# Optimization experiments

Hardware: AMD Instinct MI355X
Metric: run time of the kernel (lower is better)

Reference implementation:

```python
import jax, jax.numpy as jnp
import numpy as np

NTYPES = 4
RCUT = 6.0
MIXED_TYPES = False
BOX = 40.0  # Angstrom, sets realistic atomic density


def setup_inputs() -> dict:
    key = jax.random.key(0)
    k1, k2 = jax.random.split(key)
    nframes, nloc = 2, 4096
    coord = jax.random.uniform(k1, (nframes, nloc * 3), dtype=jnp.float32) * BOX
    atype = jax.random.randint(k2, (nframes, nloc), 0, NTYPES, dtype=jnp.int32)
    return {"coord": coord, "atype": atype}


def reference(coord, atype):
    # cell=None branch: extended coords == local coords, nall == nloc
    nframes = coord.shape[0]
    c = coord.reshape(nframes, -1, 3)              # (f, nloc, 3)
    nloc = c.shape[1]
    # diff[f, i, j] = coord[j] - coord[i], shape (f, nloc, nall, 3)
    diff = c[:, None, :, :] - c[:, :, None, :]
    rr2 = jnp.sum(diff * diff, axis=-1)            # (f, nloc, nall)
    # mask self-pairs with inf (torch sets diff rows to inf before squaring)
    eye = jnp.eye(nloc, dtype=bool)
    rr2 = jnp.where(eye[None, :, :], jnp.inf, rr2)
    min_rr2 = jnp.min(rr2, axis=-1)                # (f, nloc)
    mask = rr2 < RCUT ** 2                         # (f, nloc, nall)
    if not MIXED_TYPES:
        # per-type neighbor counts via one-hot contraction (replaces the
        # Python loop over ntypes in the torch code; same math)
        onehot = jax.nn.one_hot(atype, NTYPES, dtype=jnp.int32)  # (f, nall, t)
        nnei = jnp.einsum('fij,fjt->fit', mask.astype(jnp.int32), onehot)
    else:
        valid = (atype >= 0)[:, None, :]
        nnei = jnp.sum(mask & valid, axis=-1).astype(jnp.int32)[..., None]
    max_nnei = jnp.max(nnei, axis=1)               # (f, ntypes) or (f, 1)
    return min_rr2, max_nnei
```

## Files before the change

kernel.cpp:

```cpp
#include <hip/hip_runtime.h>
#include <stdint.h>

#define NFRAMES 2
#define NT 4
#define BLK 256
#define NJ 64

__global__ __launch_bounds__(BLK) void ns_init_kernel(unsigned* __restrict__ out_bits,
                                                      unsigned* __restrict__ ws, int n) {
    int idx = blockIdx.x * BLK + threadIdx.x;
    if (idx < n) {
        out_bits[idx] = 0x7F800000u;
        ws[idx] = 0u;
    }
}

template <bool SELFCHK>
__device__ __forceinline__ void do_pair(const float* __restrict__ cf,
                                        const int* __restrict__ tf,
                                        int j, int i,
                                        float xi, float yi, float zi,
                                        float& mm, unsigned& cc) {
#pragma clang fp contract(off)
    float dx = cf[3 * j]     - xi;
    float dy = cf[3 * j + 1] - yi;
    float dz = cf[3 * j + 2] - zi;
    unsigned sval = 1u << (tf[j] * 8);
    float xx = dx * dx;
    float yy = dy * dy;
    float zz = dz * dz;
    float r2 = (xx + yy) + zz;
    bool self = SELFCHK && (j == i);
    float rm = self ? __builtin_inff() : r2;
    mm = fminf(mm, rm);
    bool near = (r2 < 36.0f) && !self;
    cc += near ? sval : 0u;
}

__global__ __launch_bounds__(BLK) void ns_pair_kernel(const float* __restrict__ coord,
                                                      const int* __restrict__ atype,
                                                      unsigned* __restrict__ out_min_bits,
                                                      unsigned* __restrict__ ws_cnt,
                                                      int nloc) {
    const int f = blockIdx.z;
    const int ibase = blockIdx.y * BLK;
    const int i = ibase + threadIdx.x;
    const int jslice = nloc / NJ;
    const int jbase = blockIdx.x * jslice;

    const float* cf = coord + (size_t)f * nloc * 3;
    const int*   tf = atype + (size_t)f * nloc;

    const float xi = cf[3 * i];
    const float yi = cf[3 * i + 1];
    const float zi = cf[3 * i + 2];

    float m0 = __builtin_inff(), m1 = __builtin_inff();
    unsigned c0 = 0u, c1 = 0u;

    const bool overlap = (jbase >= ibase) && (jbase < ibase + BLK);

    if (overlap) {
#pragma unroll 8
        for (int j = jbase; j < jbase + jslice; j += 2) {
            do_pair<true>(cf, tf, j,     i, xi, yi, zi, m0, c0);
            do_pair<true>(cf, tf, j + 1, i, xi, yi, zi, m1, c1);
        }
    } else {
#pragma unroll 8
        for (int j = jbase; j < jbase + jslice; j += 2) {
            do_pair<false>(cf, tf, j,     i, xi, yi, zi, m0, c0);
            do_pair<false>(cf, tf, j + 1, i, xi, yi, zi, m1, c1);
        }
    }

    float minr2 = fminf(m0, m1);
    unsigned c = c0 + c1;

    atomicMin(&out_min_bits[(size_t)f * nloc + i], __float_as_uint(minr2));
    atomicAdd(&ws_cnt[(size_t)f * nloc + i], c);
}

__global__ __launch_bounds__(BLK) void ns_max_kernel(const unsigned* __restrict__ ws_cnt,
                                                     float* __restrict__ out,
                                                     int nloc) {
    const int f = blockIdx.x;
    int m0 = 0, m1 = 0, m2 = 0, m3 = 0;
    for (int i = threadIdx.x; i < nloc; i += BLK) {
        unsigned c = ws_cnt[(size_t)f * nloc + i];
        m0 = max(m0, (int)(c & 255u));
        m1 = max(m1, (int)((c >> 8) & 255u));
        m2 = max(m2, (int)((c >> 16) & 255u));
        m3 = max(m3, (int)(c >> 24));
    }
    for (int off = 32; off > 0; off >>= 1) {
        m0 = max(m0, __shfl_xor(m0, off, 64));
        m1 = max(m1, __shfl_xor(m1, off, 64));
        m2 = max(m2, __shfl_xor(m2, off, 64));
        m3 = max(m3, __shfl_xor(m3, off, 64));
    }
    __shared__ int red[BLK / 64][NT];
    int wid = threadIdx.x >> 6;
    if ((threadIdx.x & 63) == 0) {
        red[wid][0] = m0; red[wid][1] = m1; red[wid][2] = m2; red[wid][3] = m3;
    }
    __syncthreads();
    if (threadIdx.x < NT) {
        int t = threadIdx.x;
        int m = max(max(red[0][t], red[1][t]), max(red[2][t], red[3][t]));
        out[(size_t)NFRAMES * nloc + f * NT + t] = (float)m;
    }
}

extern "C" void kernel_launch(void* const* d_in, const int* in_sizes, int n_in,
                              void* d_out, int out_size, void* d_ws, size_t ws_size,
                              hipStream_t stream) {
    const float* coord = (const float*)d_in[0];
    const int*   atype = (const int*)d_in[1];
    const int nloc = in_sizes[1] / NFRAMES;

    float*    out = (float*)d_out;
    unsigned* ws  = (unsigned*)d_ws;

    const int n = NFRAMES * nloc;

    ns_init_kernel<<<(n + BLK - 1) / BLK, BLK, 0, stream>>>((unsigned*)out, ws, n);

    dim3 grid(NJ, nloc / BLK, NFRAMES);
    ns_pair_kernel<<<grid, dim3(BLK), 0, stream>>>(coord, atype, (unsigned*)out, ws, nloc);

    ns_max_kernel<<<NFRAMES, BLK, 0, stream>>>(ws, out, nloc);
}
```

Measured before the change: 27.56 us.

## Replace atomic accumulation with per-slice partial buffers and a parallel finalize

The pair kernel now writes each j-slice's partial min and packed per-type count to a workspace array instead of doing atomicMin/atomicAdd into the output. The init kernel goes away, and a new finalize kernel with one block per 256 atoms reduces the 64 partials, writes min_rr2 and per-block type maxima. A tiny last kernel reduces those block maxima. This removes atomic contention and the init launch and spreads the max reduction over more blocks, at the cost of a 4 MB partial buffer that is written and then read back, plus an extra launch.

```diff
diff --git a/kernel.cpp b/kernel.cpp
--- a/kernel.cpp
+++ b/kernel.cpp
@@ -5,15 +5,6 @@
 #define NT 4
 #define BLK 256
 #define NJ 64
-
-__global__ __launch_bounds__(BLK) void ns_init_kernel(unsigned* __restrict__ out_bits,
-                                                      unsigned* __restrict__ ws, int n) {
-    int idx = blockIdx.x * BLK + threadIdx.x;
-    if (idx < n) {
-        out_bits[idx] = 0x7F800000u;
-        ws[idx] = 0u;
-    }
-}
 
 template <bool SELFCHK>
 __device__ __forceinline__ void do_pair(const float* __restrict__ cf,
@@ -39,14 +30,14 @@
 
 __global__ __launch_bounds__(BLK) void ns_pair_kernel(const float* __restrict__ coord,
                                                       const int* __restrict__ atype,
-                                                      unsigned* __restrict__ out_min_bits,
-                                                      unsigned* __restrict__ ws_cnt,
+                                                      uint2* __restrict__ part,
                                                       int nloc) {
     const int f = blockIdx.z;
     const int ibase = blockIdx.y * BLK;
     const int i = ibase + threadIdx.x;
     const int jslice = nloc / NJ;
-    const int jbase = blockIdx.x * jslice;
+    const int jb = blockIdx.x;
+    const int jbase = jb * jslice;
 
     const float* cf = coord + (size_t)f * nloc * 3;
     const int*   tf = atype + (size_t)f * nloc;
@@ -77,22 +68,33 @@
     float minr2 = fminf(m0, m1);
     unsigned c = c0 + c1;
 
-    atomicMin(&out_min_bits[(size_t)f * nloc + i], __float_as_uint(minr2));
-    atomicAdd(&ws_cnt[(size_t)f * nloc + i], c);
+    part[((size_t)jb * NFRAMES + f) * nloc + i] =
+        make_uint2(__float_as_uint(minr2), c);
 }
 
-__global__ __launch_bounds__(BLK) void ns_max_kernel(const unsigned* __restrict__ ws_cnt,
-                                                     float* __restrict__ out,
-                                                     int nloc) {
-    const int f = blockIdx.x;
-    int m0 = 0, m1 = 0, m2 = 0, m3 = 0;
-    for (int i = threadIdx.x; i < nloc; i += BLK) {
-        unsigned c = ws_cnt[(size_t)f * nloc + i];
-        m0 = max(m0, (int)(c & 255u));
-        m1 = max(m1, (int)((c >> 8) & 255u));
-        m2 = max(m2, (int)((c >> 16) & 255u));
-        m3 = max(m3, (int)(c >> 24));
+__global__ __launch_bounds__(BLK) void ns_finalize_kernel(const uint2* __restrict__ part,
+                                                          float* __restrict__ out,
+                                                          int* __restrict__ pmax,
+                                                          int nloc) {
+    const int nbpf = nloc / BLK;
+    const int f  = blockIdx.x / nbpf;
+    const int ib = blockIdx.x % nbpf;
+    const int i  = ib * BLK + threadIdx.x;
+
+    float m = __builtin_inff();
+    unsigned c = 0u;
+#pragma unroll 16
+    for (int jb = 0; jb < NJ; ++jb) {
+        uint2 v = part[((size_t)jb * NFRAMES + f) * nloc + i];
+        m = fminf(m, __uint_as_float(v.x));
+        c += v.y;
     }
+    out[(size_t)f * nloc + i] = m;
+
+    int m0 = (int)(c & 255u);
+    int m1 = (int)((c >> 8) & 255u);
+    int m2 = (int)((c >> 16) & 255u);
+    int m3 = (int)(c >> 24);
     for (int off = 32; off > 0; off >>= 1) {
         m0 = max(m0, __shfl_xor(m0, off, 64));
         m1 = max(m1, __shfl_xor(m1, off, 64));
@@ -107,8 +109,21 @@
     __syncthreads();
     if (threadIdx.x < NT) {
         int t = threadIdx.x;
-        int m = max(max(red[0][t], red[1][t]), max(red[2][t], red[3][t]));
-        out[(size_t)NFRAMES * nloc + f * NT + t] = (float)m;
+        pmax[blockIdx.x * NT + t] =
+            max(max(red[0][t], red[1][t]), max(red[2][t], red[3][t]));
+    }
+}
+
+__global__ __launch_bounds__(64) void ns_max_kernel(const int* __restrict__ pmax,
+                                                    float* __restrict__ out,
+                                                    int nbpf, int nloc) {
+    const int t = threadIdx.x;
+    if (t < NFRAMES * NT) {
+        const int f = t / NT, tt = t % NT;
+        int m = 0;
+        for (int b = 0; b < nbpf; ++b)
+            m = max(m, pmax[(f * nbpf + b) * NT + tt]);
+        out[(size_t)NFRAMES * nloc + f * NT + tt] = (float)m;
     }
 }
 
@@ -119,15 +134,15 @@
     const int*   atype = (const int*)d_in[1];
     const int nloc = in_sizes[1] / NFRAMES;
 
-    float*    out = (float*)d_out;
-    unsigned* ws  = (unsigned*)d_ws;
-
-    const int n = NFRAMES * nloc;
-
-    ns_init_kernel<<<(n + BLK - 1) / BLK, BLK, 0, stream>>>((unsigned*)out, ws, n);
+    float* out = (float*)d_out;
+    uint2* part = (uint2*)d_ws;
+    int*   pmax = (int*)((char*)d_ws + (size_t)NJ * NFRAMES * nloc * sizeof(uint2));
 
     dim3 grid(NJ, nloc / BLK, NFRAMES);
-    ns_pair_kernel<<<grid, dim3(BLK), 0, stream>>>(coord, atype, (unsigned*)out, ws, nloc);
+    ns_pair_kernel<<<grid, dim3(BLK), 0, stream>>>(coord, atype, part, nloc);
 
-    ns_max_kernel<<<NFRAMES, BLK, 0, stream>>>(ws, out, nloc);
+    const int nbpf = nloc / BLK;
+    ns_finalize_kernel<<<NFRAMES * nbpf, BLK, 0, stream>>>(part, out, pmax, nloc);
+
+    ns_max_kernel<<<1, 64, 0, stream>>>(pmax, out, nbpf, nloc);
 }
```

After: 27.51 us. No clear change (-0.2%).
